# Kernel tuning notes

Hardware: AMD Instinct MI355X
Metric: run time of the kernel (lower is better)

The kernel has to match this reference:

```python
import jax, jax.numpy as jnp
import numpy as np

BS = 32  # block size
LN_EPS = 1e-5  # torch LayerNorm default

def setup_inputs() -> dict:
    key = jax.random.key(0)
    ks = jax.random.split(key, 6)
    B, N, D = 4, 8192, 1024
    scale = 1.0 / np.sqrt(D)
    return {
        "x": jax.random.normal(ks[0], (B, N, D), dtype=jnp.float32),
        "w_w": jax.random.normal(ks[1], (D, 1), dtype=jnp.float32) * scale,
        "w_b": jax.random.normal(ks[2], (1,), dtype=jnp.float32) * 0.01,
        "proj_w": jax.random.normal(ks[3], (3 * D, D), dtype=jnp.float32) * (1.0 / np.sqrt(3 * D)),
        "proj_b": jax.random.normal(ks[4], (D,), dtype=jnp.float32) * 0.01,
        "ln_g": jnp.ones((D,), dtype=jnp.float32),
        "ln_b": jnp.zeros((D,), dtype=jnp.float32),
        "pos": jax.random.normal(ks[5], (16384, D), dtype=jnp.float32),
    }

def reference(x, w_w, w_b, proj_w, proj_b, ln_g, ln_b, pos):
    B, N, D = x.shape
    pad = (BS - N % BS) % BS
    if pad:
        x = jnp.pad(x, ((0, 0), (0, pad), (0, 0)))
    nb = x.shape[1] // BS
    blk = x.reshape(B, nb, BS, D)
    # softmax attention weights within each block
    logits = (blk @ w_w).squeeze(-1) + w_b[0]           # [B, nb, BS]
    wt = jax.nn.softmax(logits, axis=-1)
    # softmax-weighted mean and std over the block axis
    mn = jnp.einsum('bnk,bnkd->bnd', wt, blk)           # [B, nb, D]
    var = jnp.einsum('bnk,bnkd->bnd', wt, (blk - mn[:, :, None, :]) ** 2)
    sd = jnp.sqrt(var + 1e-8)
    mx = blk.max(axis=2)                                 # [B, nb, D]
    feat = jnp.concatenate([mn, sd, mx], axis=-1)       # [B, nb, 3D]
    h = feat @ proj_w + proj_b                           # [B, nb, D]
    mu = h.mean(axis=-1, keepdims=True)
    v = ((h - mu) ** 2).mean(axis=-1, keepdims=True)
    h = (h - mu) / jnp.sqrt(v + LN_EPS) * ln_g + ln_b
    return h + pos[:nb]
```

## Files before the change

kernel.cpp:

```cpp
#include <hip/hip_runtime.h>
#include <hip/hip_bf16.h>

typedef unsigned short u16;
typedef unsigned int u32;
typedef __attribute__((ext_vector_type(4))) float f32x4;
typedef __attribute__((ext_vector_type(8))) short bf16x8;

#define DD 1024
#define BSZ 32
#define MROWS 1024
#define K3 3072
#define SPLITK 4
#define KSPLIT 768
#define BMT 128
#define BKT 64

static __device__ __forceinline__ u16 bf16rne(float f) {
    union { float f; u32 u; } a; a.f = f;
    u32 r = a.u + 0x7fffu + ((a.u >> 16) & 1u);
    return (u16)(r >> 16);
}
static __device__ __forceinline__ u32 packbf2(float a, float b) {
    return (u32)bf16rne(a) | ((u32)bf16rne(b) << 16);
}

__global__ void k_blockstats(const float* __restrict__ x, const float* __restrict__ w_w,
                             const float* __restrict__ w_b, u16* __restrict__ feat) {
    const int m = blockIdx.x;
    const int t = threadIdx.x;
    const int lane = t & 63, wv = t >> 6;
    __shared__ float lg[BSZ][8];
    __shared__ float wts[BSZ];
    const float2 wp = *(const float2*)(w_w + 2 * t);
    const float* xb = x + (size_t)m * BSZ * DD;
    float2 xs[BSZ];
#pragma unroll
    for (int r = 0; r < BSZ; ++r) {
        float2 v = *(const float2*)(xb + (size_t)r * DD + 2 * t);
        xs[r] = v;
        float d = v.x * wp.x + v.y * wp.y;
#pragma unroll
        for (int off = 32; off; off >>= 1) d += __shfl_xor(d, off);
        if (lane == 0) lg[r][wv] = d;
    }
    __syncthreads();
    if (t < BSZ) {
        float s = w_b[0];
#pragma unroll
        for (int w = 0; w < 8; ++w) s += lg[t][w];
        float mx = s;
#pragma unroll
        for (int off = 16; off; off >>= 1) mx = fmaxf(mx, __shfl_xor(mx, off, 32));
        float e = __expf(s - mx);
        float se = e;
#pragma unroll
        for (int off = 16; off; off >>= 1) se += __shfl_xor(se, off, 32);
        wts[t] = e / se;
    }
    __syncthreads();
    float wmx = 0.f, wmy = 0.f, m2x = 0.f, m2y = 0.f, mxx = -3.4e38f, mxy = -3.4e38f;
#pragma unroll
    for (int r = 0; r < BSZ; ++r) {
        float w = wts[r];
        float2 v = xs[r];
        wmx += w * v.x; wmy += w * v.y;
        m2x += w * v.x * v.x; m2y += w * v.y * v.y;
        mxx = fmaxf(mxx, v.x); mxy = fmaxf(mxy, v.y);
    }
    float sdx = sqrtf(fmaxf(m2x - wmx * wmx, 0.f) + 1e-8f);
    float sdy = sqrtf(fmaxf(m2y - wmy * wmy, 0.f) + 1e-8f);
    u32* fr = (u32*)(feat + (size_t)m * K3);
    fr[t] = packbf2(wmx, wmy);
    fr[512 + t] = packbf2(sdx, sdy);
    fr[1024 + t] = packbf2(mxx, mxy);
}

__global__ void k_transpose(const float* __restrict__ pw, u16* __restrict__ bt) {
    __shared__ float tile[64][33];
    const int bk = blockIdx.x;
    const int bn = blockIdx.y;
    const int t = threadIdx.x;
    const int c = t & 31;
    const int r0 = t >> 5;
#pragma unroll
    for (int p = 0; p < 8; ++p) {
        int r = r0 + p * 8;
        tile[r][c] = pw[(size_t)(bk * 64 + r) * DD + bn * 32 + c];
    }
    __syncthreads();
#pragma unroll
    for (int p = 0; p < 4; ++p) {
        int rr = r0 + p * 8;
        u32 u = packbf2(tile[2 * c][rr], tile[2 * c + 1][rr]);
        ((u32*)(bt + (size_t)(bn * 32 + rr) * K3 + bk * 64))[c] = u;
    }
}

__global__ __launch_bounds__(256) void k_gemm(const u16* __restrict__ A, const u16* __restrict__ Bt,
                                              float* __restrict__ part) {
    __shared__ u16 As[2][BMT * BKT];
    __shared__ u16 Bs[2][BMT * BKT];
    const int t = threadIdx.x;
    const int m0 = blockIdx.x * BMT;
    const int n0 = blockIdx.y * BMT;
    const int z = blockIdx.z;
    const int k0 = z * KSPLIT;

    const int lane = t & 63;
    const int wv = t >> 6;
    const int wm = (wv >> 1) * 64;
    const int wn = (wv & 1) * 64;
    const int l15 = lane & 15;
    const int lh = lane >> 4;

    const int srow = t >> 3;
    const int scb = (t & 7) * 16;
    const int gcb = scb ^ ((srow & 7) << 4);
    const u16* gAr = A + (size_t)(m0 + srow) * K3 + (gcb >> 1) + k0;
    const u16* gBr = Bt + (size_t)(n0 + srow) * K3 + (gcb >> 1) + k0;
    const int ldsBase = (t & ~63) * 8;

    f32x4 acc[4][4] = {};

#define STAGE(buf, kEl)                                                                            \
    {                                                                                              \
        _Pragma("unroll") for (int j = 0; j < 4; ++j) {                                            \
            __builtin_amdgcn_global_load_lds(                                                      \
                (__attribute__((address_space(1))) void*)(gAr + (kEl) + (size_t)j * 32 * K3),      \
                (__attribute__((address_space(3))) void*)&As[buf][j * 2048 + ldsBase], 16, 0, 0);  \
            __builtin_amdgcn_global_load_lds(                                                      \
                (__attribute__((address_space(1))) void*)(gBr + (kEl) + (size_t)j * 32 * K3),      \
                (__attribute__((address_space(3))) void*)&Bs[buf][j * 2048 + ldsBase], 16, 0, 0);  \
        }                                                                                          \
    }
#define LDIDX(row, cb) ((((row)*128) + (((cb) ^ (((row)&7) << 4)))) >> 1)

    STAGE(0, 0)
    __syncthreads();
    int cur = 0;
    for (int it = 0; it < KSPLIT / BKT; ++it) {
        if (it < KSPLIT / BKT - 1) STAGE(cur ^ 1, (it + 1) * BKT)
#pragma unroll
        for (int kk = 0; kk < 2; ++kk) {
            bf16x8 af[4], bfr[4];
            const int cb = kk * 64 + lh * 16;
#pragma unroll
            for (int mi = 0; mi < 4; ++mi)
                af[mi] = *(const bf16x8*)&As[cur][LDIDX(wm + mi * 16 + l15, cb)];
#pragma unroll
            for (int ni = 0; ni < 4; ++ni)
                bfr[ni] = *(const bf16x8*)&Bs[cur][LDIDX(wn + ni * 16 + l15, cb)];
#pragma unroll
            for (int mi = 0; mi < 4; ++mi)
#pragma unroll
                for (int ni = 0; ni < 4; ++ni)
                    acc[mi][ni] =
                        __builtin_amdgcn_mfma_f32_16x16x32_bf16(af[mi], bfr[ni], acc[mi][ni], 0, 0, 0);
        }
        __syncthreads();
        cur ^= 1;
    }

    float* pz = part + (size_t)z * MROWS * DD;
#pragma unroll
    for (int mi = 0; mi < 4; ++mi) {
#pragma unroll
        for (int r = 0; r < 4; ++r) {
            const int gm = m0 + wm + mi * 16 + lh * 4 + r;
            float* rp = pz + (size_t)gm * DD + n0 + wn + l15;
#pragma unroll
            for (int ni = 0; ni < 4; ++ni) rp[ni * 16] = acc[mi][ni][r];
        }
    }
#undef STAGE
#undef LDIDX
}

__global__ void k_lnreduce(const float* __restrict__ part, const float* __restrict__ proj_b,
                           const float* __restrict__ ln_g, const float* __restrict__ ln_b,
                           const float* __restrict__ pos, float* __restrict__ out) {
    const int m = blockIdx.x;
    const int t = threadIdx.x;
    const int c = 4 * t;
    const int lane = t & 63, wv = t >> 6;
    f32x4 h = {};
#pragma unroll
    for (int s = 0; s < SPLITK; ++s)
        h += *(const f32x4*)(part + ((size_t)s * MROWS + m) * DD + c);
    h += *(const f32x4*)(proj_b + c);
    float sm = h[0] + h[1] + h[2] + h[3];
    float sq = h[0] * h[0] + h[1] * h[1] + h[2] * h[2] + h[3] * h[3];
#pragma unroll
    for (int off = 32; off; off >>= 1) { sm += __shfl_xor(sm, off); sq += __shfl_xor(sq, off); }
    __shared__ float rs[4], rq[4];
    if (lane == 0) { rs[wv] = sm; rq[wv] = sq; }
    __syncthreads();
    const float S = rs[0] + rs[1] + rs[2] + rs[3];
    const float Q = rq[0] + rq[1] + rq[2] + rq[3];
    const float mu = S * (1.f / 1024.f);
    const float var = Q * (1.f / 1024.f) - mu * mu;
    const float rstd = rsqrtf(var + 1e-5f);
    const f32x4 g = *(const f32x4*)(ln_g + c);
    const f32x4 b = *(const f32x4*)(ln_b + c);
    const f32x4 p = *(const f32x4*)(pos + (size_t)(m & 255) * DD + c);
    f32x4 o;
#pragma unroll
    for (int i = 0; i < 4; ++i) o[i] = (h[i] - mu) * rstd * g[i] + b[i] + p[i];
    *(f32x4*)(out + (size_t)m * DD + c) = o;
}

extern "C" void kernel_launch(void* const* d_in, const int* in_sizes, int n_in,
                              void* d_out, int out_size, void* d_ws, size_t ws_size,
                              hipStream_t stream) {
    const float* x      = (const float*)d_in[0];
    const float* w_w    = (const float*)d_in[1];
    const float* w_b    = (const float*)d_in[2];
    const float* proj_w = (const float*)d_in[3];
    const float* proj_b = (const float*)d_in[4];
    const float* ln_g   = (const float*)d_in[5];
    const float* ln_b   = (const float*)d_in[6];
    const float* pos    = (const float*)d_in[7];
    float* out = (float*)d_out;

    char* ws = (char*)d_ws;
    u16* feat  = (u16*)ws;
    u16* bt    = (u16*)(ws + 6291456);
    float* prt = (float*)(ws + 12582912);

    k_blockstats<<<1024, 512, 0, stream>>>(x, w_w, w_b, feat);
    k_transpose<<<dim3(48, 32), 256, 0, stream>>>(proj_w, bt);
    k_gemm<<<dim3(8, 8, SPLITK), 256, 0, stream>>>(feat, bt, prt);
    k_lnreduce<<<1024, 256, 0, stream>>>(prt, proj_b, ln_g, ln_b, pos, out);
}
```

Before: 274.1 us.

## Merge block-stats and weight transpose into one launch with vectorized loads

```diff
diff --git a/kernel.cpp b/kernel.cpp
--- a/kernel.cpp
+++ b/kernel.cpp
@@ -4,6 +4,7 @@
 typedef unsigned short u16;
 typedef unsigned int u32;
 typedef __attribute__((ext_vector_type(4))) float f32x4;
+typedef __attribute__((ext_vector_type(4))) unsigned int u32x4;
 typedef __attribute__((ext_vector_type(8))) short bf16x8;
 
 #define DD 1024
@@ -24,75 +25,83 @@
     return (u32)bf16rne(a) | ((u32)bf16rne(b) << 16);
 }
 
-__global__ void k_blockstats(const float* __restrict__ x, const float* __restrict__ w_w,
-                             const float* __restrict__ w_b, u16* __restrict__ feat) {
-    const int m = blockIdx.x;
+__global__ __launch_bounds__(512, 1) void k_prep(const float* __restrict__ x,
+                                                 const float* __restrict__ w_w,
+                                                 const float* __restrict__ w_b,
+                                                 u16* __restrict__ feat,
+                                                 const float* __restrict__ pw,
+                                                 u16* __restrict__ bt) {
+    __shared__ float smem[64 * 68];
     const int t = threadIdx.x;
-    const int lane = t & 63, wv = t >> 6;
-    __shared__ float lg[BSZ][8];
-    __shared__ float wts[BSZ];
-    const float2 wp = *(const float2*)(w_w + 2 * t);
-    const float* xb = x + (size_t)m * BSZ * DD;
-    float2 xs[BSZ];
-#pragma unroll
-    for (int r = 0; r < BSZ; ++r) {
-        float2 v = *(const float2*)(xb + (size_t)r * DD + 2 * t);
-        xs[r] = v;
-        float d = v.x * wp.x + v.y * wp.y;
-#pragma unroll
-        for (int off = 32; off; off >>= 1) d += __shfl_xor(d, off);
-        if (lane == 0) lg[r][wv] = d;
-    }
-    __syncthreads();
-    if (t < BSZ) {
-        float s = w_b[0];
-#pragma unroll
-        for (int w = 0; w < 8; ++w) s += lg[t][w];
-        float mx = s;
-#pragma unroll
-        for (int off = 16; off; off >>= 1) mx = fmaxf(mx, __shfl_xor(mx, off, 32));
-        float e = __expf(s - mx);
-        float se = e;
-#pragma unroll
-        for (int off = 16; off; off >>= 1) se += __shfl_xor(se, off, 32);
-        wts[t] = e / se;
-    }
-    __syncthreads();
-    float wmx = 0.f, wmy = 0.f, m2x = 0.f, m2y = 0.f, mxx = -3.4e38f, mxy = -3.4e38f;
-#pragma unroll
-    for (int r = 0; r < BSZ; ++r) {
-        float w = wts[r];
-        float2 v = xs[r];
-        wmx += w * v.x; wmy += w * v.y;
-        m2x += w * v.x * v.x; m2y += w * v.y * v.y;
-        mxx = fmaxf(mxx, v.x); mxy = fmaxf(mxy, v.y);
-    }
-    float sdx = sqrtf(fmaxf(m2x - wmx * wmx, 0.f) + 1e-8f);
-    float sdy = sqrtf(fmaxf(m2y - wmy * wmy, 0.f) + 1e-8f);
-    u32* fr = (u32*)(feat + (size_t)m * K3);
-    fr[t] = packbf2(wmx, wmy);
-    fr[512 + t] = packbf2(sdx, sdy);
-    fr[1024 + t] = packbf2(mxx, mxy);
-}
-
-__global__ void k_transpose(const float* __restrict__ pw, u16* __restrict__ bt) {
-    __shared__ float tile[64][33];
-    const int bk = blockIdx.x;
-    const int bn = blockIdx.y;
-    const int t = threadIdx.x;
-    const int c = t & 31;
-    const int r0 = t >> 5;
-#pragma unroll
-    for (int p = 0; p < 8; ++p) {
-        int r = r0 + p * 8;
-        tile[r][c] = pw[(size_t)(bk * 64 + r) * DD + bn * 32 + c];
-    }
-    __syncthreads();
-#pragma unroll
-    for (int p = 0; p < 4; ++p) {
-        int rr = r0 + p * 8;
-        u32 u = packbf2(tile[2 * c][rr], tile[2 * c + 1][rr]);
-        ((u32*)(bt + (size_t)(bn * 32 + rr) * K3 + bk * 64))[c] = u;
+    if (blockIdx.x < 1024) {
+        const int m = blockIdx.x;
+        const int lane = t & 63, wv = t >> 6;
+        const float2 wp = *(const float2*)(w_w + 2 * t);
+        const float* xb = x + (size_t)m * (BSZ * DD);
+        float2 xs[BSZ];
+#pragma unroll
+        for (int r = 0; r < BSZ; ++r)
+            xs[r] = *(const float2*)(xb + (size_t)r * DD + 2 * t);
+#pragma unroll
+        for (int r = 0; r < BSZ; ++r) {
+            float d = xs[r].x * wp.x + xs[r].y * wp.y;
+            d += __shfl_xor(d, 1); d += __shfl_xor(d, 2); d += __shfl_xor(d, 4);
+            if ((lane & 7) == 0) smem[r * 68 + wv * 8 + (lane >> 3)] = d;
+        }
+        __syncthreads();
+        float* wts = smem + 32 * 68;
+        if (t < 32) {
+            float s = w_b[0];
+            const float* row = smem + t * 68;
+#pragma unroll
+            for (int j = 0; j < 16; ++j) {
+                f32x4 v = *(const f32x4*)(row + 4 * j);
+                s += v[0] + v[1] + v[2] + v[3];
+            }
+            float mx = s;
+#pragma unroll
+            for (int off = 16; off; off >>= 1) mx = fmaxf(mx, __shfl_xor(mx, off, 32));
+            float e = __expf(s - mx);
+            float se = e;
+#pragma unroll
+            for (int off = 16; off; off >>= 1) se += __shfl_xor(se, off, 32);
+            wts[t] = e / se;
+        }
+        __syncthreads();
+        float wmx = 0.f, wmy = 0.f, m2x = 0.f, m2y = 0.f, mxx = -3.4e38f, mxy = -3.4e38f;
+#pragma unroll
+        for (int r = 0; r < BSZ; ++r) {
+            float w = wts[r];
+            float2 v = xs[r];
+            wmx += w * v.x; wmy += w * v.y;
+            m2x += w * v.x * v.x; m2y += w * v.y * v.y;
+            mxx = fmaxf(mxx, v.x); mxy = fmaxf(mxy, v.y);
+        }
+        float sdx = sqrtf(fmaxf(m2x - wmx * wmx, 0.f) + 1e-8f);
+        float sdy = sqrtf(fmaxf(m2y - wmy * wmy, 0.f) + 1e-8f);
+        u32* fr = (u32*)(feat + (size_t)m * K3);
+        fr[t] = packbf2(wmx, wmy);
+        fr[512 + t] = packbf2(sdx, sdy);
+        fr[1024 + t] = packbf2(mxx, mxy);
+    } else {
+        const int bid = blockIdx.x - 1024;
+        const int bk = bid >> 4;
+        const int bn = bid & 15;
+        const int r = t >> 3;
+        const int c0 = (t & 7) * 8;
+        const float* src = pw + (size_t)(bk * 64 + r) * DD + bn * 64 + c0;
+        float4 v0 = *(const float4*)(src);
+        float4 v1 = *(const float4*)(src + 4);
+        *(float4*)(smem + r * 68 + c0) = v0;
+        *(float4*)(smem + r * 68 + c0 + 4) = v1;
+        __syncthreads();
+        const int n = t >> 3;
+        const int kq = (t & 7) * 8;
+        u32x4 o;
+#pragma unroll
+        for (int j = 0; j < 4; ++j)
+            o[j] = packbf2(smem[(kq + 2 * j) * 68 + n], smem[(kq + 2 * j + 1) * 68 + n]);
+        *(u32x4*)(bt + (size_t)(bn * 64 + n) * K3 + bk * 64 + kq) = o;
     }
 }
 
@@ -227,8 +236,7 @@
     u16* bt    = (u16*)(ws + 6291456);
     float* prt = (float*)(ws + 12582912);
 
-    k_blockstats<<<1024, 512, 0, stream>>>(x, w_w, w_b, feat);
-    k_transpose<<<dim3(48, 32), 256, 0, stream>>>(proj_w, bt);
+    k_prep<<<1792, 512, 0, stream>>>(x, w_w, w_b, feat, proj_w, bt);
     k_gemm<<<dim3(8, 8, SPLITK), 256, 0, stream>>>(feat, bt, prt);
     k_lnreduce<<<1024, 256, 0, stream>>>(prt, proj_b, ln_g, ln_b, pos, out);
 }
```

After: 259.8 us. -5.2%, faster.
